# Optimization experiments

Measured on AMD Instinct MI355X. Metric: run time of the kernel, lower is better.

Reference implementation:

```python
import jax, jax.numpy as jnp
import numpy as np

GROUP = 4      # number of groups in the batch dim
SHARED_GP = 4  # conv groups for q/k 1x1 convs
C = 512
N = 4096
B = 4          # B_all = GROUP * B = 16
EPS_LN = 1e-6
EPS_Z = 1e-6


def _phi(x):
    return jax.nn.relu(x) + 1.0


def _grouped_1x1(x, W):
    # x: [B, C, N], W: [g, C/g, C/g] block-diagonal 1x1 conv weights
    Bx, Cx, Nx = x.shape
    g = W.shape[0]
    xg = x.reshape(Bx, g, Cx // g, Nx)
    return jnp.einsum('goc,bgcn->bgon', W, xg).reshape(Bx, Cx, Nx)


def _ln(x, w, b, eps=EPS_LN):
    m = jnp.mean(x, axis=-1, keepdims=True)
    v = jnp.mean(jnp.square(x - m), axis=-1, keepdims=True)
    return (x - m) * jax.lax.rsqrt(v + eps) * w + b


def setup_inputs() -> dict:
    key = jax.random.key(0)
    ks = jax.random.split(key, 12)
    cg = C // SHARED_GP
    s = 1.0 / np.sqrt(C)
    return {
        'x': jax.random.normal(ks[0], (GROUP * B, C, N), dtype=jnp.float32),
        'Wq': jax.random.normal(ks[1], (SHARED_GP, cg, cg), dtype=jnp.float32) / np.sqrt(cg),
        'Wk': jax.random.normal(ks[2], (SHARED_GP, cg, cg), dtype=jnp.float32) / np.sqrt(cg),
        'Wv': jax.random.normal(ks[3], (C, C), dtype=jnp.float32) * s,
        'Wphi': jax.random.normal(ks[4], (C, C), dtype=jnp.float32) * s,
        'ln1_w': jnp.ones((C,), dtype=jnp.float32),
        'ln1_b': jnp.zeros((C,), dtype=jnp.float32),
        'fc1_w': jax.random.normal(ks[5], (4 * C, C), dtype=jnp.float32) * s,
        'fc1_b': jnp.zeros((4 * C,), dtype=jnp.float32),
        'fc2_w': jax.random.normal(ks[6], (C, 4 * C), dtype=jnp.float32) / np.sqrt(4 * C),
        'fc2_b': jnp.zeros((C,), dtype=jnp.float32),
        'ln2_w': jnp.ones((C,), dtype=jnp.float32),
        'ln2_b': jnp.zeros((C,), dtype=jnp.float32),
    }


def reference(x, Wq, Wk, Wv, Wphi, ln1_w, ln1_b, fc1_w, fc1_b, fc2_w, fc2_b, ln2_w, ln2_b):
    B_all, Cc, Nn = x.shape
    g = GROUP
    Bb = B_all // g
    first, rest = x[:Bb], x[Bb:]             # [B,C,N], [M,C,N] with M=(g-1)*B
    M = (g - 1) * Bb

    q = _phi(_grouped_1x1(rest, Wq))          # [M,C,N]
    k0 = _phi(_grouped_1x1(first, Wk))        # [B,C,N]
    v0 = jnp.einsum('oc,bcn->bon', Wv, first)  # [B,C,N]
    phi_first = jnp.einsum('oc,bcn->bon', Wphi, first)
    phi_rest = jnp.einsum('oc,bcn->bon', Wphi, rest)

    # expand first-group k/v across the (g-1) query groups
    k = jnp.broadcast_to(k0[None], (g - 1, Bb, Cc, Nn)).reshape(M, Cc, Nn)
    v = jnp.broadcast_to(v0[None], (g - 1, Bb, Cc, Nn)).reshape(M, Cc, Nn)

    Qg = jnp.broadcast_to(k0.mean(axis=2, keepdims=True)[None],
                          (g - 1, Bb, Cc, 1)).reshape(M, Cc, 1)
    alpha = jax.nn.softmax(jnp.sum(Qg * k, axis=1, keepdims=True), axis=-1) * Nn  # [M,1,N]
    k_hat = k * alpha

    # linear attention: kv = k_hat @ v^T / sqrt(C)
    kv = jnp.einsum('mcn,mdn->mcd', k_hat, v) / jnp.sqrt(jnp.asarray(Cc, x.dtype))  # [M,C,C]
    k_sum = jnp.sum(k_hat, axis=-1)                                  # [M,C]
    z = 1.0 / (jnp.einsum('mcn,mc->mn', q, k_sum)[:, None, :] + EPS_Z)  # [M,1,N]
    y = jnp.einsum('mcn,mcd->mdn', q, kv) * z * phi_rest              # [M,C,N]

    y_first = jnp.mean(y, axis=0, keepdims=True) * phi_first          # [B,C,N]
    out_first = _ln((first + y_first).transpose(0, 2, 1), ln1_w, ln1_b)  # [B,N,C]
    h = jax.nn.relu(out_first @ fc1_w.T + fc1_b)
    out_first = out_first + h @ fc2_w.T + fc2_b
    out_first = jax.nn.relu(_ln(out_first, ln2_w, ln2_b))
    out_first = out_first.transpose(0, 2, 1)                          # [B,C,N]
    return jnp.concatenate([out_first, rest], axis=0)
```

## Files before the change

### kernel.cpp

```cpp
#include <hip/hip_runtime.h>

#define N_DIM 4096
#define C_DIM 512
#define CN_ ((long)C_DIM * (long)N_DIM)

typedef unsigned short ushort_t;
typedef __attribute__((ext_vector_type(8))) short bf16x8;
typedef __attribute__((ext_vector_type(4))) float f32x4;

typedef const __attribute__((address_space(1))) unsigned int* gas_t;
typedef __attribute__((address_space(3))) unsigned int* las_t;
#define GLOAD(g, l) __builtin_amdgcn_global_load_lds((gas_t)(g), (las_t)(l), 16, 0, 0)

__device__ __forceinline__ ushort_t f2b(float f) {
    unsigned u = __builtin_bit_cast(unsigned, f);
    u += 0x7fffu + ((u >> 16) & 1u);
    return (ushort_t)(u >> 16);
}
__device__ __forceinline__ float b2f(ushort_t s) {
    return __builtin_bit_cast(float, (unsigned)s << 16);
}

enum { EPI_NONE = 0, EPI_PHI = 1, EPI_RELU_BIAS = 2, EPI_RES_BIAS = 3, EPI_PRE = 4 };

#define STAGE(q, koff) { \
    GLOAD(ap0 + (koff), &Als[q][la0]); \
    GLOAD(ap1 + (koff), &Als[q][la1]); \
    GLOAD(bp0 + (koff), &Bls[q][la0]); \
    GLOAD(bp1 + (koff), &Bls[q][la1]); }

#define COMPUTE(q) { \
    bf16x8 af[4], bfv[4]; \
    _Pragma("unroll") for (int m_ = 0; m_ < 4; ++m_) \
        af[m_] = *(const bf16x8*)&Als[q][(wr + m_ * 16 + fr) * 32 + rsw]; \
    _Pragma("unroll") for (int nf_ = 0; nf_ < 4; ++nf_) \
        bfv[nf_] = *(const bf16x8*)&Bls[q][(wc + nf_ * 16 + fr) * 32 + rsw]; \
    _Pragma("unroll") for (int m_ = 0; m_ < 4; ++m_) \
        _Pragma("unroll") for (int nf_ = 0; nf_ < 4; ++nf_) \
            acc[m_][nf_] = __builtin_amdgcn_mfma_f32_16x16x32_bf16( \
                af[m_], bfv[nf_], acc[m_][nf_], 0, 0, 0); }

#define KLOOP(K_) { \
    STAGE(0, 0); \
    __syncthreads(); \
    int kk_ = 0; \
    while (true) { \
        if (kk_ + 32 < (K_)) STAGE(1, kk_ + 32); \
        COMPUTE(0); \
        __syncthreads(); \
        kk_ += 32; \
        if (kk_ >= (K_)) break; \
        if (kk_ + 32 < (K_)) STAGE(0, kk_ + 32); \
        COMPUTE(1); \
        __syncthreads(); \
        kk_ += 32; \
        if (kk_ >= (K_)) break; \
    } }

template<int EPI, bool GROUPED, bool OBF, bool DEN, bool QGS>
__global__ __launch_bounds__(256, 3) void mfma_gemm(
    const ushort_t* __restrict__ Wb, const ushort_t* __restrict__ A,
    void* __restrict__ OUTV, const float* __restrict__ bias,
    const ushort_t* __restrict__ auxb, const float* __restrict__ auxf,
    int K, int O, int a_rstride, long a_zstride, long o_zstride, long auxb_zstride,
    int xt, int yt)
{
    __shared__ ushort_t Als[2][128 * 32];
    __shared__ ushort_t Bls[2][128 * 32];
    const int tid = threadIdx.x;

    const int L = blockIdx.x;
    const int gpx = (gridDim.x >> 3) / xt;
    const int xcd = L & 7;
    const int j = L >> 3;
    const int xtile = j % xt;
    const int g = xcd * gpx + j / xt;
    const int ytile = g % yt;
    const int z = g / yt;

    const int o0 = xtile * 128;
    const int n0 = ytile * 128;
    const ushort_t* Az = A + (long)z * a_zstride;
    const ushort_t* Wp = Wb;
    int kbase = 0, obase = o0;
    if (GROUPED) { int gg = o0 >> 7; Wp = Wb + (long)gg * (128 * 128); kbase = gg << 7; obase = 0; }

    const int w = tid >> 6, l = tid & 63;
    const int lr = l >> 2, lg = l & 3;
    const int rA0 = w * 32 + lr, rA1 = w * 32 + 16 + lr;
    const int gA0 = lg ^ ((rA0 >> 1) & 3), gA1 = lg ^ ((rA1 >> 1) & 3);
    const ushort_t* ap0 = Az + (long)(n0 + rA0) * a_rstride + kbase + gA0 * 8;
    const ushort_t* ap1 = Az + (long)(n0 + rA1) * a_rstride + kbase + gA1 * 8;
    const ushort_t* bp0 = Wp + (long)(obase + rA0) * K + gA0 * 8;
    const ushort_t* bp1 = Wp + (long)(obase + rA1) * K + gA1 * 8;
    const int la0 = (w * 32) * 32, la1 = (w * 32 + 16) * 32;

    const int wr = (w >> 1) * 64, wc = (w & 1) * 64;
    const int fr = l & 15, ks = l >> 4;
    const int rsw = (ks ^ ((fr >> 1) & 3)) << 3;

    f32x4 acc[4][4];
#pragma unroll
    for (int m = 0; m < 4; ++m)
#pragma unroll
        for (int nf = 0; nf < 4; ++nf) acc[m][nf] = f32x4{0.f, 0.f, 0.f, 0.f};

    KLOOP(K);

    float dsum[4][4];
    if (DEN) {
#pragma unroll
        for (int m = 0; m < 4; ++m)
#pragma unroll
            for (int j2 = 0; j2 < 4; ++j2) dsum[m][j2] = 0.f;
    }
    float qsum[4];
    if (QGS) {
#pragma unroll
        for (int nf = 0; nf < 4; ++nf) qsum[nf] = 0.f;
    }

#pragma unroll
    for (int m = 0; m < 4; ++m) {
#pragma unroll
        for (int nf = 0; nf < 4; ++nf) {
            const int oo = o0 + wc + nf * 16 + fr;
            float bval = 0.f;
            if (EPI == EPI_RELU_BIAS || EPI == EPI_RES_BIAS) bval = bias[oo];
            float kw = 0.f;
            if (DEN) kw = bias[((z & 3) << 9) + oo];
#pragma unroll
            for (int j2 = 0; j2 < 4; ++j2) {
                const int nn = n0 + wr + m * 16 + ks * 4 + j2;
                const long ridx = (long)nn * O + oo;
                float v = acc[m][nf][j2];
                if (EPI == EPI_PHI)            v = fmaxf(v, 0.f) + 1.f;
                else if (EPI == EPI_RELU_BIAS) v = fmaxf(v + bval, 0.f);
                else if (EPI == EPI_RES_BIAS)  v = v + bval + b2f(auxb[(long)z * auxb_zstride + ridx]);
                else if (EPI == EPI_PRE)       v = b2f(auxb[(long)z * auxb_zstride + ridx]) + auxf[ridx] * v;
                if (DEN) dsum[m][j2] += v * kw;
                if (QGS) qsum[nf] += v;
                if (OBF) ((ushort_t*)OUTV)[(long)z * o_zstride + ridx] = f2b(v);
                else     ((float*)OUTV)[(long)z * o_zstride + ridx] = v;
            }
        }
    }

    if (DEN) {
#pragma unroll
        for (int m = 0; m < 4; ++m)
#pragma unroll
            for (int j2 = 0; j2 < 4; ++j2) {
                float d = dsum[m][j2];
                d += __shfl_xor(d, 1); d += __shfl_xor(d, 2);
                d += __shfl_xor(d, 4); d += __shfl_xor(d, 8);
                if (fr == 0) {
                    const int nn = n0 + wr + m * 16 + ks * 4 + j2;
                    atomicAdd((float*)&auxf[(long)z * N_DIM + nn], d);
                }
            }
    }
    if (QGS) {
#pragma unroll
        for (int nf = 0; nf < 4; ++nf) {
            float d = qsum[nf];
            d += __shfl_xor(d, 16);
            d += __shfl_xor(d, 32);
            if (ks == 0) {
                const int oo = o0 + wc + nf * 16 + fr;
                atomicAdd((float*)&auxf[((long)z << 9) + oo], d);
            }
        }
    }
}

__global__ __launch_bounds__(256, 3) void kv_mfma(
    const ushort_t* __restrict__ v0c, const ushort_t* __restrict__ khat,
    float* __restrict__ kvp)
{
    __shared__ ushort_t Als[2][128 * 32];
    __shared__ ushort_t Bls[2][128 * 32];
    const int tid = threadIdx.x;
    const int L = blockIdx.x;
    const int gpx = (gridDim.x >> 3) >> 2;
    const int xcd = L & 7;
    const int j = L >> 3;
    const int xtile = j & 3;
    const int g = xcd * gpx + (j >> 2);
    const int ytile = g & 3;
    const int z = g >> 2;
    const int c0 = xtile * 128, d0 = ytile * 128;
    const int b = z >> 3, nch = z & 7;

    const int w = tid >> 6, l = tid & 63;
    const int lr = l >> 2, lg = l & 3;
    const int rA0 = w * 32 + lr, rA1 = w * 32 + 16 + lr;
    const int gA0 = lg ^ ((rA0 >> 1) & 3), gA1 = lg ^ ((rA1 >> 1) & 3);
    const ushort_t* Ab = v0c + (long)b * CN_ + nch * 512;
    const ushort_t* Bb = khat + (long)b * CN_ + nch * 512;
    const ushort_t* ap0 = Ab + (long)(d0 + rA0) * N_DIM + gA0 * 8;
    const ushort_t* ap1 = Ab + (long)(d0 + rA1) * N_DIM + gA1 * 8;
    const ushort_t* bp0 = Bb + (long)(c0 + rA0) * N_DIM + gA0 * 8;
    const ushort_t* bp1 = Bb + (long)(c0 + rA1) * N_DIM + gA1 * 8;
    const int la0 = (w * 32) * 32, la1 = (w * 32 + 16) * 32;

    const int wr = (w >> 1) * 64, wc = (w & 1) * 64;
    const int fr = l & 15, ks = l >> 4;
    const int rsw = (ks ^ ((fr >> 1) & 3)) << 3;

    f32x4 acc[4][4];
#pragma unroll
    for (int m = 0; m < 4; ++m)
#pragma unroll
        for (int nf = 0; nf < 4; ++nf) acc[m][nf] = f32x4{0.f, 0.f, 0.f, 0.f};

    KLOOP(512);

    float* KV = kvp + ((long)(nch * 4 + b)) * 262144;
#pragma unroll
    for (int m = 0; m < 4; ++m)
#pragma unroll
        for (int nf = 0; nf < 4; ++nf) {
            const int cc = c0 + wc + nf * 16 + fr;
#pragma unroll
            for (int j2 = 0; j2 < 4; ++j2) {
                const int dd = d0 + wr + m * 16 + ks * 4 + j2;
                KV[(long)dd * 512 + cc] = acc[m][nf][j2];
            }
        }
}

__global__ __launch_bounds__(256) void cvt_scale8(
    const float* __restrict__ kvp, ushort_t* __restrict__ out)
{
    const float s = 0.044194173824159216f;
    const long i = ((long)blockIdx.x * 256 + threadIdx.x) * 4;
    const int b = (int)(i >> 18);
    const long j = i & 262143;
    float4 a = make_float4(0.f, 0.f, 0.f, 0.f);
#pragma unroll
    for (int nch = 0; nch < 8; ++nch) {
        float4 v = *(const float4*)&kvp[((long)(nch * 4 + b)) * 262144 + j];
        a.x += v.x; a.y += v.y; a.z += v.z; a.w += v.w;
    }
    union { ushort_t sh[4]; uint2 u; } p;
    p.sh[0] = f2b(a.x * s); p.sh[1] = f2b(a.y * s);
    p.sh[2] = f2b(a.z * s); p.sh[3] = f2b(a.w * s);
    *(uint2*)&out[i] = p.u;
}

__global__ __launch_bounds__(256, 2) void ybar_gemm(
    const ushort_t* __restrict__ q12, const ushort_t* __restrict__ kvT,
    const ushort_t* __restrict__ xT12, const ushort_t* __restrict__ Wphi_b,
    const float* __restrict__ den12, ushort_t* __restrict__ y12)
{
    __shared__ ushort_t Als[2][128 * 32];
    __shared__ ushort_t Bls[2][128 * 32];
    const int tid = threadIdx.x;
    const int L = blockIdx.x;
    const int gpx = (gridDim.x >> 3) >> 2;
    const int xcd = L & 7;
    const int j = L >> 3;
    const int xtile = j & 3;
    const int g = xcd * gpx + (j >> 2);
    const int ytile = g & 31;
    const int mm = g >> 5;
    const int o0 = xtile * 128, n0 = ytile * 128;

    const int w = tid >> 6, l = tid & 63;
    const int lr = l >> 2, lg = l & 3;
    const int rA0 = w * 32 + lr, rA1 = w * 32 + 16 + lr;
    const int gA0 = lg ^ ((rA0 >> 1) & 3), gA1 = lg ^ ((rA1 >> 1) & 3);
    const long aoff0 = (long)(n0 + rA0) * 512 + gA0 * 8;
    const long aoff1 = (long)(n0 + rA1) * 512 + gA1 * 8;
    const long boff0 = (long)(o0 + rA0) * 512 + gA0 * 8;
    const long boff1 = (long)(o0 + rA1) * 512 + gA1 * 8;
    const int la0 = (w * 32) * 32, la1 = (w * 32 + 16) * 32;

    const int wr = (w >> 1) * 64, wc = (w & 1) * 64;
    const int fr = l & 15, ks = l >> 4;
    const int rsw = (ks ^ ((fr >> 1) & 3)) << 3;

    f32x4 acc[4][4];
#pragma unroll
    for (int m = 0; m < 4; ++m)
#pragma unroll
        for (int nf = 0; nf < 4; ++nf) acc[m][nf] = f32x4{0.f, 0.f, 0.f, 0.f};

    const ushort_t* ap0 = xT12 + (long)mm * CN_ + aoff0;
    const ushort_t* ap1 = xT12 + (long)mm * CN_ + aoff1;
    const ushort_t* bp0 = Wphi_b + boff0;
    const ushort_t* bp1 = Wphi_b + boff1;
    KLOOP(512);

    uint2 ph[4][4];
#pragma unroll
    for (int m = 0; m < 4; ++m)
#pragma unroll
        for (int nf = 0; nf < 4; ++nf) {
            ph[m][nf].x = (unsigned)f2b(acc[m][nf][0]) | ((unsigned)f2b(acc[m][nf][1]) << 16);
            ph[m][nf].y = (unsigned)f2b(acc[m][nf][2]) | ((unsigned)f2b(acc[m][nf][3]) << 16);
            acc[m][nf] = f32x4{0.f, 0.f, 0.f, 0.f};
        }

    ap0 = q12 + (long)mm * CN_ + aoff0;
    ap1 = q12 + (long)mm * CN_ + aoff1;
    bp0 = kvT + (long)(mm & 3) * 262144 + boff0;
    bp1 = kvT + (long)(mm & 3) * 262144 + boff1;
    KLOOP(512);

    const float* D = den12 + (long)mm * N_DIM;
    ushort_t* Y = y12 + (long)mm * CN_;
#pragma unroll
    for (int m = 0; m < 4; ++m) {
        float zr[4];
#pragma unroll
        for (int j2 = 0; j2 < 4; ++j2)
            zr[j2] = 1.f / (D[n0 + wr + m * 16 + ks * 4 + j2] + 1e-6f);
#pragma unroll
        for (int nf = 0; nf < 4; ++nf) {
            const int oo = o0 + wc + nf * 16 + fr;
            float pv[4];
            pv[0] = b2f((ushort_t)(ph[m][nf].x & 0xffff));
            pv[1] = b2f((ushort_t)(ph[m][nf].x >> 16));
            pv[2] = b2f((ushort_t)(ph[m][nf].y & 0xffff));
            pv[3] = b2f((ushort_t)(ph[m][nf].y >> 16));
#pragma unroll
            for (int j2 = 0; j2 < 4; ++j2) {
                const int nn = n0 + wr + m * 16 + ks * 4 + j2;
                Y[(long)nn * 512 + oo] = f2b(acc[m][nf][j2] * zr[j2] * pv[j2]);
            }
        }
    }
}

__global__ __launch_bounds__(256) void ybar_reduce(
    const ushort_t* __restrict__ y12, float* __restrict__ ybar)
{
    const long i = ((long)blockIdx.x * 256 + threadIdx.x) * 8;
    float s[8] = {0.f, 0.f, 0.f, 0.f, 0.f, 0.f, 0.f, 0.f};
    for (int mm = 0; mm < 12; ++mm) {
        uint4 u = *(const uint4*)&y12[(long)mm * CN_ + i];
        const ushort_t* us = (const ushort_t*)&u;
#pragma unroll
        for (int j = 0; j < 8; ++j) s[j] += b2f(us[j]);
    }
#pragma unroll
    for (int j = 0; j < 8; ++j) s[j] *= (1.f / 12.f);
    *(float4*)&ybar[i] = make_float4(s[0], s[1], s[2], s[3]);
    *(float4*)&ybar[i + 4] = make_float4(s[4], s[5], s[6], s[7]);
}

template<int ALPHA>
__global__ __launch_bounds__(256) void transpose_b2b(
    const ushort_t* __restrict__ in, ushort_t* __restrict__ out,
    const float* __restrict__ alpha, float* __restrict__ ksum)
{
    __shared__ ushort_t t[64][72];
    const int tid = threadIdx.x;
    const int n0 = blockIdx.x * 64, c0 = blockIdx.y * 64, z = blockIdx.z;
    const ushort_t* I = in + (long)z * CN_;
    ushort_t* O = out + (long)z * CN_;
    const int r = tid >> 2, s8 = (tid & 3) * 16;
    uint4 u0 = *(const uint4*)&I[(long)(n0 + r) * 512 + c0 + s8];
    uint4 u1 = *(const uint4*)&I[(long)(n0 + r) * 512 + c0 + s8 + 8];
    *(uint4*)&t[r][s8] = u0;
    *(uint4*)&t[r][s8 + 8] = u1;
    __syncthreads();
    union { ushort_t sh[16]; uint4 u[2]; } p;
#pragma unroll
    for (int i = 0; i < 16; ++i) {
        ushort_t v = t[s8 + i][r];
        if (ALPHA) v = f2b(b2f(v) * alpha[(long)z * N_DIM + n0 + s8 + i]);
        p.sh[i] = v;
    }
    uint4* dst = (uint4*)&O[(long)(c0 + r) * N_DIM + n0 + s8];
    dst[0] = p.u[0]; dst[1] = p.u[1];
    if (ALPHA) {
        const int c = tid & 63, q = tid >> 6;
        float s = 0.f;
#pragma unroll
        for (int i = 0; i < 16; ++i) {
            const int n = q * 16 + i;
            s += b2f(t[n][c]) * alpha[(long)z * N_DIM + n0 + n];
        }
        atomicAdd(&ksum[((long)z << 9) + c0 + c], s);
    }
}

__global__ __launch_bounds__(256) void cvt_all(
    const float* __restrict__ s0, ushort_t* __restrict__ d0,
    const float* __restrict__ s1, ushort_t* __restrict__ d1,
    const float* __restrict__ s2, ushort_t* __restrict__ d2,
    const float* __restrict__ s3, ushort_t* __restrict__ d3,
    const float* __restrict__ s4, ushort_t* __restrict__ d4,
    const float* __restrict__ s5, ushort_t* __restrict__ d5)
{
    long i = ((long)blockIdx.x * 256 + threadIdx.x) * 4;
    const float* s; ushort_t* d; long off;
    if (i < 65536)        { s = s0; d = d0; off = i; }
    else if (i < 131072)  { s = s1; d = d1; off = i - 65536; }
    else if (i < 393216)  { s = s2; d = d2; off = i - 131072; }
    else if (i < 655360)  { s = s3; d = d3; off = i - 393216; }
    else if (i < 1703936) { s = s4; d = d4; off = i - 655360; }
    else                  { s = s5; d = d5; off = i - 1703936; }
    float4 v = *(const float4*)&s[off];
    union { ushort_t sh[4]; uint2 u; } p;
    p.sh[0] = f2b(v.x); p.sh[1] = f2b(v.y); p.sh[2] = f2b(v.z); p.sh[3] = f2b(v.w);
    *(uint2*)&d[off] = p.u;
}

template<int PASSZ>
__global__ __launch_bounds__(256) void transpose_f2b(
    const float* __restrict__ in, ushort_t* __restrict__ out,
    int rows, int cols, long in_z, long out_z, float* __restrict__ passout)
{
    __shared__ float t[64][65];
    const int tid = threadIdx.x;
    const int n0 = blockIdx.x * 64, c0 = blockIdx.y * 64;
    const int z = blockIdx.z;
    const float* I = in + (long)z * in_z;
    ushort_t* Ot = out + (long)z * out_z;
    const int r = tid >> 2, s4 = (tid & 3) * 16;
    float4 raw[4];
#pragma unroll
    for (int i = 0; i < 16; i += 4) {
        float4 v = *(const float4*)&I[(long)(c0 + r) * cols + n0 + s4 + i];
        raw[i >> 2] = v;
        t[r][s4 + i] = v.x; t[r][s4 + i + 1] = v.y;
        t[r][s4 + i + 2] = v.z; t[r][s4 + i + 3] = v.w;
    }
    if (PASSZ && z >= 4) {
        float* P = passout + (long)z * in_z + (long)(c0 + r) * cols + n0 + s4;
#pragma unroll
        for (int i = 0; i < 4; ++i) *(float4*)&P[i * 4] = raw[i];
    }
    __syncthreads();
    union { ushort_t s[16]; uint4 u[2]; } pk;
#pragma unroll
    for (int i = 0; i < 16; ++i) pk.s[i] = f2b(t[s4 + i][r]);
    uint4* dst = (uint4*)&Ot[(long)(n0 + r) * rows + c0 + s4];
    dst[0] = pk.u[0]; dst[1] = pk.u[1];
}

__global__ __launch_bounds__(256) void dot_rows(
    const ushort_t* __restrict__ X, const float* __restrict__ w,
    float* __restrict__ out, float scale)
{
    const int tid = threadIdx.x;
    const int rn = tid >> 2, cs = (tid & 3) * 128;
    const int z = blockIdx.y;
    const int n = blockIdx.x * 64 + rn;
    const ushort_t* row = X + (long)z * CN_ + (long)n * C_DIM;
    const float* wz = w + (long)(z & 3) * C_DIM;
    float s = 0.f;
    for (int i = 0; i < 128; i += 8) {
        uint4 u = *(const uint4*)&row[cs + i];
        const ushort_t* us = (const ushort_t*)&u;
#pragma unroll
        for (int k2 = 0; k2 < 8; ++k2) s += b2f(us[k2]) * wz[cs + i + k2];
    }
    s += __shfl_xor(s, 1); s += __shfl_xor(s, 2);
    if ((tid & 3) == 0) out[(long)z * N_DIM + n] = s * scale;
}

__global__ __launch_bounds__(256) void softmax_alpha(
    const float* __restrict__ logits, float* __restrict__ alpha)
{
    int b = blockIdx.x, tid = threadIdx.x;
    const float* L = logits + (long)b * N_DIM;
    float* A = alpha + (long)b * N_DIM;
    float lv[16];
    float mx = -3.4e38f;
#pragma unroll
    for (int i = 0; i < 4; i++) {
        float4 v = *(const float4*)&L[tid * 4 + i * 1024];
        lv[4 * i + 0] = v.x; lv[4 * i + 1] = v.y; lv[4 * i + 2] = v.z; lv[4 * i + 3] = v.w;
        mx = fmaxf(mx, fmaxf(fmaxf(v.x, v.y), fmaxf(v.z, v.w)));
    }
    __shared__ float red[8];
    float m = mx;
#pragma unroll
    for (int off = 32; off; off >>= 1) m = fmaxf(m, __shfl_down(m, off, 64));
    int wid = tid >> 6, lane = tid & 63;
    if (lane == 0) red[wid] = m;
    __syncthreads();
    m = fmaxf(fmaxf(red[0], red[1]), fmaxf(red[2], red[3]));
    float e[16], s = 0.f;
#pragma unroll
    for (int i = 0; i < 16; i++) { e[i] = expf(lv[i] - m); s += e[i]; }
#pragma unroll
    for (int off = 32; off; off >>= 1) s += __shfl_down(s, off, 64);
    if (lane == 0) red[4 + wid] = s;
    __syncthreads();
    float S = red[4] + red[5] + red[6] + red[7];
    float sc = 4096.f / S;
#pragma unroll
    for (int i = 0; i < 4; i++)
        *(float4*)&A[tid * 4 + i * 1024] =
            make_float4(e[4 * i] * sc, e[4 * i + 1] * sc, e[4 * i + 2] * sc, e[4 * i + 3] * sc);
}

template<int RELU, int OBF, int IBF>
__global__ __launch_bounds__(256) void ln_row(
    const void* __restrict__ inv, const float* __restrict__ g,
    const float* __restrict__ bt, void* __restrict__ outv)
{
    const int tid = threadIdx.x;
    const int r = tid >> 3, cs = (tid & 7) * 64;
    const long base = (((long)blockIdx.y * N_DIM) + blockIdx.x * 32 + r) * C_DIM + cs;
    float vv[64];
    float s = 0.f, s2 = 0.f;
    if (IBF) {
        const ushort_t* I = (const ushort_t*)inv + base;
#pragma unroll
        for (int i = 0; i < 8; ++i) {
            uint4 u = *(const uint4*)&I[i * 8];
            const ushort_t* us = (const ushort_t*)&u;
#pragma unroll
            for (int jj = 0; jj < 8; ++jj) {
                float f = b2f(us[jj]); vv[i * 8 + jj] = f; s += f; s2 += f * f;
            }
        }
    } else {
        const float* I = (const float*)inv + base;
#pragma unroll
        for (int i = 0; i < 16; ++i) {
            float4 v = *(const float4*)&I[i * 4];
            vv[i * 4] = v.x; vv[i * 4 + 1] = v.y; vv[i * 4 + 2] = v.z; vv[i * 4 + 3] = v.w;
            s += v.x + v.y + v.z + v.w;
            s2 += v.x * v.x + v.y * v.y + v.z * v.z + v.w * v.w;
        }
    }
#pragma unroll
    for (int off = 1; off < 8; off <<= 1) { s += __shfl_xor(s, off); s2 += __shfl_xor(s2, off); }
    const float mean = s * (1.f / 512.f);
    const float var = s2 * (1.f / 512.f) - mean * mean;
    const float rs = rsqrtf(var + 1e-6f);
#pragma unroll
    for (int i = 0; i < 64; i += 4) {
        float o[4];
#pragma unroll
        for (int jj = 0; jj < 4; ++jj) {
            float ov = (vv[i + jj] - mean) * rs * g[cs + i + jj] + bt[cs + i + jj];
            if (RELU) ov = fmaxf(ov, 0.f);
            o[jj] = ov;
        }
        if (OBF) {
            union { ushort_t s4[4]; uint2 u; } p;
            p.s4[0] = f2b(o[0]); p.s4[1] = f2b(o[1]); p.s4[2] = f2b(o[2]); p.s4[3] = f2b(o[3]);
            *(uint2*)&((ushort_t*)outv)[base + i] = p.u;
        } else {
            *(float4*)&((float*)outv)[base + i] = make_float4(o[0], o[1], o[2], o[3]);
        }
    }
}

__global__ __launch_bounds__(256) void ln_tr(
    const ushort_t* __restrict__ in, const float* __restrict__ g,
    const float* __restrict__ bt, float* __restrict__ out)
{
    __shared__ float t[32][513];
    const int tid = threadIdx.x;
    const int r = tid >> 3;
    const int lc = (tid & 7) * 8;
    const int z = blockIdx.y;
    const long n = (long)blockIdx.x * 32 + r;
    const ushort_t* I = in + ((long)z * N_DIM + n) * C_DIM;
    float vv[64];
    float s = 0.f, s2 = 0.f;
#pragma unroll
    for (int i = 0; i < 8; ++i) {
        const int c = i * 64 + lc;
        uint4 u = *(const uint4*)&I[c];
        const ushort_t* us = (const ushort_t*)&u;
#pragma unroll
        for (int jj = 0; jj < 8; ++jj) {
            float f = b2f(us[jj]); vv[i * 8 + jj] = f; s += f; s2 += f * f;
        }
    }
#pragma unroll
    for (int off = 1; off < 8; off <<= 1) { s += __shfl_xor(s, off); s2 += __shfl_xor(s2, off); }
    const float mean = s * (1.f / 512.f);
    const float var = s2 * (1.f / 512.f) - mean * mean;
    const float rs = rsqrtf(var + 1e-6f);
#pragma unroll
    for (int i = 0; i < 8; ++i) {
        const int c = i * 64 + lc;
#pragma unroll
        for (int jj = 0; jj < 8; ++jj) {
            float o = (vv[i * 8 + jj] - mean) * rs * g[c + jj] + bt[c + jj];
            t[r][c + jj] = fmaxf(o, 0.f);
        }
    }
    __syncthreads();
    float* O = out + (long)z * CN_ + (long)blockIdx.x * 32;
    for (int c = tid; c < 512; c += 256) {
        float* dst = O + (long)c * N_DIM;
#pragma unroll
        for (int i = 0; i < 32; i += 4)
            *(float4*)&dst[i] = make_float4(t[i][c], t[i + 1][c], t[i + 2][c], t[i + 3][c]);
    }
}

extern "C" void kernel_launch(void* const* d_in, const int* in_sizes, int n_in,
                              void* d_out, int out_size, void* d_ws, size_t ws_size,
                              hipStream_t stream)
{
    const float* x     = (const float*)d_in[0];
    const float* Wq    = (const float*)d_in[1];
    const float* Wk    = (const float*)d_in[2];
    const float* Wv    = (const float*)d_in[3];
    const float* Wphi  = (const float*)d_in[4];
    const float* ln1_w = (const float*)d_in[5];
    const float* ln1_b = (const float*)d_in[6];
    const float* fc1_w = (const float*)d_in[7];
    const float* fc1_bias = (const float*)d_in[8];
    const float* fc2_w = (const float*)d_in[9];
    const float* fc2_bias = (const float*)d_in[10];
    const float* ln2_w = (const float*)d_in[11];
    const float* ln2_b = (const float*)d_in[12];
    float* out = (float*)d_out;

    float* ws = (float*)d_ws;
    const long CN = CN_;
    ushort_t* xTfirst = (ushort_t*)ws;
    ushort_t* tln     = (ushort_t*)ws;
    ushort_t* xT12 = (ushort_t*)(ws + 2 * CN);
    ushort_t* hbuf4 = (ushort_t*)(ws + 2 * CN);
    ushort_t* q12   = (ushort_t*)(ws + 8 * CN);
    ushort_t* y12   = (ushort_t*)(ws + 14 * CN);
    ushort_t* k0b = (ushort_t*)(ws + 20 * CN);
    ushort_t* v0b = (ushort_t*)(ws + 22 * CN);
    ushort_t* pre_b = (ushort_t*)(ws + 20 * CN);
    ushort_t* khat = (ushort_t*)(ws + 24 * CN);
    ushort_t* v0c  = (ushort_t*)(ws + 26 * CN);
    ushort_t* ubuf_b = (ushort_t*)(ws + 24 * CN);
    float* ybar = ws + 32 * CN;
    float* kvp  = ws + 33 * CN;
    ushort_t* kvT = (ushort_t*)(ws + 33 * CN + 8388608);
    float* wb = ws + 33 * CN + 8388608 + 524288;
    ushort_t* Wk_b   = (ushort_t*)(wb);
    ushort_t* Wq_b   = (ushort_t*)(wb + 32768);
    ushort_t* Wv_b   = (ushort_t*)(wb + 65536);
    ushort_t* Wphi_b = (ushort_t*)(wb + 196608);
    ushort_t* fc1_b16 = (ushort_t*)(wb + 327680);
    ushort_t* fc2_b16 = (ushort_t*)(wb + 851968);
    float* Qg     = wb + 1376256;
    float* ksum   = wb + 1378304;
    float* logits = wb + 1380352;
    float* alpha  = wb + 1396736;
    float* den12  = wb + 1413120;

    dim3 blk(256);

    cvt_all<<<2688, blk, 0, stream>>>(Wk, Wk_b, Wq, Wq_b, Wv, Wv_b,
                                      Wphi, Wphi_b, fc1_w, fc1_b16, fc2_w, fc2_b16);
    hipMemsetAsync(Qg, 0, 4096 * sizeof(float), stream);
    hipMemsetAsync(den12, 0, 49152 * sizeof(float), stream);

    transpose_f2b<1><<<dim3(64, 8, 16), blk, 0, stream>>>(
        x, xTfirst, 512, 4096, CN, CN, out);

    mfma_gemm<EPI_PHI, true, true, false, true><<<512, blk, 0, stream>>>(
        Wk_b, xTfirst, k0b, nullptr, nullptr, Qg, 128, 512, 512, CN, CN, 0, 4, 32);
    mfma_gemm<EPI_NONE, false, true, false, false><<<512, blk, 0, stream>>>(
        Wv_b, xTfirst, v0b, nullptr, nullptr, nullptr, 512, 512, 512, CN, CN, 0, 4, 32);
    dot_rows<<<dim3(64, 4), blk, 0, stream>>>(k0b, Qg, logits, 1.f / 4096.f);
    softmax_alpha<<<4, blk, 0, stream>>>(logits, alpha);
    transpose_b2b<1><<<dim3(64, 8, 4), blk, 0, stream>>>(k0b, khat, alpha, ksum);
    transpose_b2b<0><<<dim3(64, 8, 4), blk, 0, stream>>>(v0b, v0c, nullptr, nullptr);
    kv_mfma<<<512, blk, 0, stream>>>(v0c, khat, kvp);
    cvt_scale8<<<1024, blk, 0, stream>>>(kvp, kvT);

    mfma_gemm<EPI_PHI, true, true, true, false><<<1536, blk, 0, stream>>>(
        Wq_b, xT12, q12, ksum, nullptr, den12, 128, 512, 512, CN, CN, 0, 4, 32);
    ybar_gemm<<<1536, blk, 0, stream>>>(q12, kvT, xT12, Wphi_b, den12, y12);
    ybar_reduce<<<1024, blk, 0, stream>>>(y12, ybar);

    mfma_gemm<EPI_PRE, false, true, false, false><<<512, blk, 0, stream>>>(
        Wphi_b, xTfirst, pre_b, nullptr, xTfirst, ybar, 512, 512, 512, CN, CN, CN, 4, 32);
    ln_row<0, 1, 1><<<dim3(128, 4), blk, 0, stream>>>(pre_b, ln1_w, ln1_b, tln);
    mfma_gemm<EPI_RELU_BIAS, false, true, false, false><<<2048, blk, 0, stream>>>(
        fc1_b16, tln, hbuf4, fc1_bias, nullptr, nullptr,
        512, 2048, 512, CN, 8388608, 0, 16, 32);
    mfma_gemm<EPI_RES_BIAS, false, true, false, false><<<512, blk, 0, stream>>>(
        fc2_b16, hbuf4, ubuf_b, fc2_bias, tln, nullptr,
        2048, 512, 2048, 8388608, CN, CN, 4, 32);
    ln_tr<<<dim3(128, 4), blk, 0, stream>>>(ubuf_b, ln2_w, ln2_b, out);
}
```

Measured before the change: 468.7 us.

## Fuse the two sequential K-loops in ybar_gemm into one interleaved loop

The phi projection GEMM and the q·kv GEMM used to run back to back, each with its own K-loop. They now share one double-buffered loop that stages all four operand tiles per step and issues MFMAs for both accumulators. This halves the number of loop iterations and barriers, and drops the bf16 rounding of the phi intermediate. In exchange it doubles LDS use (four double-buffered tiles) and accumulator registers (two 4x4 f32x4 sets), which may exceed the 2-blocks-per-SM launch bound and cause spills or lower occupancy.

```diff
diff --git a/kernel.cpp b/kernel.cpp
--- a/kernel.cpp
+++ b/kernel.cpp
@@ -256,6 +256,8 @@
 {
     __shared__ ushort_t Als[2][128 * 32];
     __shared__ ushort_t Bls[2][128 * 32];
+    __shared__ ushort_t Cls[2][128 * 32];
+    __shared__ ushort_t Dls[2][128 * 32];
     const int tid = threadIdx.x;
     const int L = blockIdx.x;
     const int gpx = (gridDim.x >> 3) >> 2;
@@ -281,33 +283,62 @@
     const int fr = l & 15, ks = l >> 4;
     const int rsw = (ks ^ ((fr >> 1) & 3)) << 3;
 
-    f32x4 acc[4][4];
+    const ushort_t* pa0 = xT12 + (long)mm * CN_ + aoff0;
+    const ushort_t* pa1 = xT12 + (long)mm * CN_ + aoff1;
+    const ushort_t* pb0 = Wphi_b + boff0;
+    const ushort_t* pb1 = Wphi_b + boff1;
+    const ushort_t* qa0 = q12 + (long)mm * CN_ + aoff0;
+    const ushort_t* qa1 = q12 + (long)mm * CN_ + aoff1;
+    const ushort_t* kb0 = kvT + (long)(mm & 3) * 262144 + boff0;
+    const ushort_t* kb1 = kvT + (long)(mm & 3) * 262144 + boff1;
+
+    f32x4 accP[4][4], accQ[4][4];
 #pragma unroll
     for (int m = 0; m < 4; ++m)
 #pragma unroll
-        for (int nf = 0; nf < 4; ++nf) acc[m][nf] = f32x4{0.f, 0.f, 0.f, 0.f};
-
-    const ushort_t* ap0 = xT12 + (long)mm * CN_ + aoff0;
-    const ushort_t* ap1 = xT12 + (long)mm * CN_ + aoff1;
-    const ushort_t* bp0 = Wphi_b + boff0;
-    const ushort_t* bp1 = Wphi_b + boff1;
-    KLOOP(512);
-
-    uint2 ph[4][4];
-#pragma unroll
-    for (int m = 0; m < 4; ++m)
-#pragma unroll
         for (int nf = 0; nf < 4; ++nf) {
-            ph[m][nf].x = (unsigned)f2b(acc[m][nf][0]) | ((unsigned)f2b(acc[m][nf][1]) << 16);
-            ph[m][nf].y = (unsigned)f2b(acc[m][nf][2]) | ((unsigned)f2b(acc[m][nf][3]) << 16);
-            acc[m][nf] = f32x4{0.f, 0.f, 0.f, 0.f};
-        }
-
-    ap0 = q12 + (long)mm * CN_ + aoff0;
-    ap1 = q12 + (long)mm * CN_ + aoff1;
-    bp0 = kvT + (long)(mm & 3) * 262144 + boff0;
-    bp1 = kvT + (long)(mm & 3) * 262144 + boff1;
-    KLOOP(512);
+            accP[m][nf] = f32x4{0.f, 0.f, 0.f, 0.f};
+            accQ[m][nf] = f32x4{0.f, 0.f, 0.f, 0.f};
+        }
+
+#define STAGE2(q, koff) { \
+    GLOAD(pa0 + (koff), &Als[q][la0]); GLOAD(pa1 + (koff), &Als[q][la1]); \
+    GLOAD(pb0 + (koff), &Bls[q][la0]); GLOAD(pb1 + (koff), &Bls[q][la1]); \
+    GLOAD(qa0 + (koff), &Cls[q][la0]); GLOAD(qa1 + (koff), &Cls[q][la1]); \
+    GLOAD(kb0 + (koff), &Dls[q][la0]); GLOAD(kb1 + (koff), &Dls[q][la1]); }
+
+#define COMPUTE2(q) { \
+    bf16x8 af[4], bfv[4], cf[4], df[4]; \
+    _Pragma("unroll") for (int m_ = 0; m_ < 4; ++m_) { \
+        af[m_] = *(const bf16x8*)&Als[q][(wr + m_ * 16 + fr) * 32 + rsw]; \
+        cf[m_] = *(const bf16x8*)&Cls[q][(wr + m_ * 16 + fr) * 32 + rsw]; } \
+    _Pragma("unroll") for (int nf_ = 0; nf_ < 4; ++nf_) { \
+        bfv[nf_] = *(const bf16x8*)&Bls[q][(wc + nf_ * 16 + fr) * 32 + rsw]; \
+        df[nf_] = *(const bf16x8*)&Dls[q][(wc + nf_ * 16 + fr) * 32 + rsw]; } \
+    _Pragma("unroll") for (int m_ = 0; m_ < 4; ++m_) \
+        _Pragma("unroll") for (int nf_ = 0; nf_ < 4; ++nf_) { \
+            accP[m_][nf_] = __builtin_amdgcn_mfma_f32_16x16x32_bf16( \
+                af[m_], bfv[nf_], accP[m_][nf_], 0, 0, 0); \
+            accQ[m_][nf_] = __builtin_amdgcn_mfma_f32_16x16x32_bf16( \
+                cf[m_], df[nf_], accQ[m_][nf_], 0, 0, 0); } }
+
+    STAGE2(0, 0);
+    __syncthreads();
+    int kk = 0;
+    while (true) {
+        if (kk + 32 < 512) STAGE2(1, kk + 32);
+        COMPUTE2(0);
+        __syncthreads();
+        kk += 32;
+        if (kk >= 512) break;
+        if (kk + 32 < 512) STAGE2(0, kk + 32);
+        COMPUTE2(1);
+        __syncthreads();
+        kk += 32;
+        if (kk >= 512) break;
+    }
+#undef STAGE2
+#undef COMPUTE2
 
     const float* D = den12 + (long)mm * N_DIM;
     ushort_t* Y = y12 + (long)mm * CN_;
@@ -320,15 +351,10 @@
 #pragma unroll
         for (int nf = 0; nf < 4; ++nf) {
             const int oo = o0 + wc + nf * 16 + fr;
-            float pv[4];
-            pv[0] = b2f((ushort_t)(ph[m][nf].x & 0xffff));
-            pv[1] = b2f((ushort_t)(ph[m][nf].x >> 16));
-            pv[2] = b2f((ushort_t)(ph[m][nf].y & 0xffff));
-            pv[3] = b2f((ushort_t)(ph[m][nf].y >> 16));
 #pragma unroll
             for (int j2 = 0; j2 < 4; ++j2) {
                 const int nn = n0 + wr + m * 16 + ks * 4 + j2;
-                Y[(long)nn * 512 + oo] = f2b(acc[m][nf][j2] * zr[j2] * pv[j2]);
+                Y[(long)nn * 512 + oo] = f2b(accQ[m][nf][j2] * zr[j2] * accP[m][nf][j2]);
             }
         }
     }
```

New measurement: 459.1 us. 1.02x faster.
